# Kernel optimization log

Measured on AMD Instinct MI355X. Metric: run time of the kernel, lower is better.

The kernel has to match this reference:

```python
import jax, jax.numpy as jnp
import numpy as np

K_NN = 64          # ume_knn
RADIUS = 1.5       # ume_desc_rad
EPS_M = 1e-6
EPS_T = 1e-16


def ball_query_idx(kp, pts, K, radius):
    # kp: [bs, n_kp, 3], pts: [bs, N, 3] -> idx [bs, n_kp, K], -1 padded
    N = pts.shape[1]
    d2 = jnp.sum((kp[:, :, None, :] - pts[:, None, :, :]) ** 2, axis=-1)  # [bs,n_kp,N]
    mask = d2 < radius ** 2
    cand = jnp.where(mask, jnp.arange(N, dtype=jnp.int32), N)
    order = jnp.sort(cand, axis=-1)[..., :K]          # first K in-ball indices (by point index)
    return jnp.where(order == N, -1, order)


def ball_query_gather(pts, idx):
    # pad row 0 with zeros so idx=-1 gathers zeros (matches torch ball_query_gather)
    bs = pts.shape[0]
    padded = jnp.concatenate([jnp.zeros((bs, 1, pts.shape[-1]), pts.dtype), pts], axis=1)
    return padded[jnp.arange(bs)[:, None, None], idx + 1]  # [bs, n_kp, K, D]


def ume_mat(points, features):
    # points: [B', K, 3], features: [B', K, F] -> [B', F, 4]
    m0 = jnp.sum(features, axis=1)                       # [B', F]
    m1 = jnp.einsum('bkf,bkd->bfd', features, points)    # [B', F, 3]
    um = jnp.concatenate([m0[:, :, None], m1], axis=2)   # [B', F, 4]
    denom = jnp.sum(m0, axis=-1)[:, None, None] + EPS_M  # [B',1,1]
    return um / denom


def batch_estimate_transform_ume(G, H):
    # G, H: [B, F, 4]
    mg, mh = G[:, :, 0:1], H[:, :, 0:1]                  # [B,F,1]
    g, h = G[:, :, 1:], H[:, :, 1:]                      # [B,F,3]
    mg_sq = jnp.sum(mg ** 2, axis=1, keepdims=True) + EPS_T
    mg_mh = jnp.sum(mg * mh, axis=1, keepdims=True)
    gmg = jnp.sum(g * mg, axis=1, keepdims=True)         # [B,1,3]
    hmg = jnp.sum(h * mg, axis=1, keepdims=True)
    wlc = gmg / (mg_sq + EPS_T)
    wrc = hmg / (mg_mh + EPS_T)
    left = g - wlc * mg
    right = h - wrc * mh
    M = jnp.einsum('bfi,bfj->bij', right, left)          # right^T @ left, [B,3,3]
    U, S, VH = jnp.linalg.svd(jnp.swapaxes(M, 1, 2))
    sgn = jnp.sign(jnp.linalg.det(U @ VH))
    qd = jnp.stack([jnp.ones_like(sgn), jnp.ones_like(sgn), sgn], axis=-1)  # diag(1,1,sgn)
    R = (U * qd[:, None, :]) @ VH                        # [B,3,3]
    b2 = (wrc - wlc @ R)[:, 0, :]                        # [B,3]
    H_orth = jnp.linalg.qr(H, mode='reduced')[0]
    G_orth = jnp.linalg.qr(G, mode='reduced')[0]
    diff = H_orth @ jnp.swapaxes(H_orth, 1, 2) - G_orth @ jnp.swapaxes(G_orth, 1, 2)
    D = 0.707 * jnp.sqrt(jnp.sum(diff ** 2, axis=(1, 2)))
    top = jnp.concatenate([jnp.swapaxes(R, 1, 2), b2[:, :, None]], axis=2)  # [B,3,4]
    bottom = jnp.broadcast_to(jnp.array([[0.0, 0.0, 0.0, 1.0]], G.dtype), (G.shape[0], 1, 4))
    T = jnp.concatenate([top, bottom], axis=1)           # [B,4,4]
    return T, D


def setup_inputs() -> dict:
    key = jax.random.key(0)
    ks = jax.random.split(key, 6)
    bs, N, F, n_kp = 2, 16384, 64, 64
    return {
        'source_points': jax.random.normal(ks[0], (bs, N, 3), jnp.float32),
        'source_features': jax.random.uniform(ks[1], (bs, N, F), jnp.float32),
        'source_kp': jax.random.normal(ks[2], (bs, n_kp, 3), jnp.float32),
        'target_points': jax.random.normal(ks[3], (bs, N, 3), jnp.float32),
        'target_features': jax.random.uniform(ks[4], (bs, N, F), jnp.float32),
        'target_kp': jax.random.normal(ks[5], (bs, n_kp, 3), jnp.float32),
    }


def reference(source_points, source_features, source_kp, target_points, target_features, target_kp):
    bs, n_kp = source_kp.shape[0], source_kp.shape[1]
    F = source_features.shape[-1]
    s_idx = ball_query_idx(source_kp, source_points, K_NN, RADIUS)
    t_idx = ball_query_idx(target_kp, target_points, K_NN, RADIUS)
    s_pts = ball_query_gather(source_points, s_idx).reshape(bs * n_kp, K_NN, 3)
    s_ft = ball_query_gather(source_features, s_idx).reshape(bs * n_kp, K_NN, F)
    t_pts = ball_query_gather(target_points, t_idx).reshape(bs * n_kp, K_NN, 3)
    t_ft = ball_query_gather(target_features, t_idx).reshape(bs * n_kp, K_NN, F)
    G_kp = ume_mat(s_pts, s_ft).reshape(bs, n_kp, F, 4)[:, :, None]   # [bs,n_kp,1,F,4]
    H_kp = ume_mat(t_pts, t_ft).reshape(bs, n_kp, F, 4)[:, None]      # [bs,1,n_kp,F,4]
    G = jnp.broadcast_to(G_kp, (bs, n_kp, n_kp, F, 4)).reshape(-1, F, 4)
    H = jnp.broadcast_to(H_kp, (bs, n_kp, n_kp, F, 4)).reshape(-1, F, 4)
    T, D = batch_estimate_transform_ume(G, H)
    T = T.reshape(bs, n_kp, n_kp, 4, 4)
    D = D.reshape(bs, n_kp, n_kp)
    return T, D, jnp.squeeze(G_kp), jnp.squeeze(H_kp)
```

## Files before the change

### kernel.cpp

```cpp
#include <hip/hip_runtime.h>
#include <math.h>

#define N_PTS 16384
#define N_KP  64
#define NF    64
#define KNN   64
#define NWAVE 16

#define OFF_T 0
#define OFF_D 131072
#define OFF_G 139264
#define OFF_H 172032

__device__ __forceinline__ float wsum(float v) {
  #pragma unroll
  for (int m = 1; m < 64; m <<= 1) v += __shfl_xor(v, m, 64);
  return v;
}

__global__ __launch_bounds__(1024) void ume_stage1(
    const float* __restrict__ sp, const float* __restrict__ sf, const float* __restrict__ skp,
    const float* __restrict__ tp, const float* __restrict__ tf, const float* __restrict__ tkp,
    float* __restrict__ out, double* __restrict__ rec)
{
  const int kp = blockIdx.x, b = blockIdx.y, side = blockIdx.z;
  const int tid  = threadIdx.x;
  const int lane = tid & 63;
  const int w    = tid >> 6;
  const float* pts  = side ? tp  : sp;
  const float* feat = side ? tf  : sf;
  const float* kps  = side ? tkp : skp;

  const float kx = kps[(b*N_KP + kp)*3 + 0];
  const float ky = kps[(b*N_KP + kp)*3 + 1];
  const float kz = kps[(b*N_KP + kp)*3 + 2];

  __shared__ int   s_widx[NWAVE*KNN];
  __shared__ int   s_wcount[NWAVE];
  __shared__ int   s_woff[NWAVE];
  __shared__ int   s_total;
  __shared__ int   s_final[KNN];
  __shared__ float s_px[KNN], s_py[KNN], s_pz[KNN];
  __shared__ float s_m0[NWAVE][NF], s_mx[NWAVE][NF], s_my[NWAVE][NF], s_mz[NWAVE][NF];

  float px[16], py[16], pz[16];
  const size_t pbase = ((size_t)b*N_PTS + w*1024 + lane)*3;
  #pragma unroll
  for (int k = 0; k < 16; ++k) {
    const float* pp = pts + pbase + (size_t)k*64*3;
    px[k] = pp[0]; py[k] = pp[1]; pz[k] = pp[2];
  }
  int running = 0;
  #pragma unroll
  for (int k = 0; k < 16; ++k) {
    const float dx = px[k]-kx, dy = py[k]-ky, dz = pz[k]-kz;
    const bool hit = (dx*dx + dy*dy + dz*dz) < 2.25f;
    const unsigned long long m = __ballot(hit);
    if (hit) {
      const int pos = running + __popcll(m & ((1ull<<lane)-1ull));
      if (pos < KNN) s_widx[w*KNN + pos] = w*1024 + k*64 + lane;
    }
    running += (int)__popcll(m);
  }
  if (lane == 0) s_wcount[w] = running > KNN ? KNN : running;
  __syncthreads();

  if (tid < NWAVE) {
    int off = 0;
    for (int q = 0; q < tid; ++q) off += s_wcount[q];
    s_woff[tid] = off;
    if (tid == NWAVE-1) {
      int tot = off + s_wcount[tid];
      s_total = tot > KNN ? KNN : tot;
    }
  }
  __syncthreads();

  {
    const int e = tid & 63, ww = tid >> 6;
    if (e < s_wcount[ww]) {
      const int slot = s_woff[ww] + e;
      if (slot < KNN) s_final[slot] = s_widx[ww*KNN + e];
    }
  }
  __syncthreads();

  const int total = s_total;
  if (tid < KNN && tid < total) {
    const float* pp = pts + ((size_t)b*N_PTS + s_final[tid])*3;
    s_px[tid] = pp[0]; s_py[tid] = pp[1]; s_pz[tid] = pp[2];
  }
  __syncthreads();

  {
    const int f = tid & 63, g = tid >> 6;
    float m0 = 0.f, mxv = 0.f, myv = 0.f, mzv = 0.f;
    for (int k = g; k < total; k += NWAVE) {
      const float fv = feat[((size_t)b*N_PTS + s_final[k])*NF + f];
      m0  += fv;
      mxv += fv * s_px[k];
      myv += fv * s_py[k];
      mzv += fv * s_pz[k];
    }
    s_m0[g][f] = m0; s_mx[g][f] = mxv; s_my[g][f] = myv; s_mz[g][f] = mzv;
  }
  __syncthreads();

  if (tid >= 64) return;

  float m0 = 0.f, mxv = 0.f, myv = 0.f, mzv = 0.f;
  #pragma unroll
  for (int g = 0; g < NWAVE; ++g) {
    m0  += s_m0[g][lane];
    mxv += s_mx[g][lane];
    myv += s_my[g][lane];
    mzv += s_mz[g][lane];
  }
  const float denom = wsum(m0) + 1e-6f;
  float u[4];
  u[0] = m0/denom; u[1] = mxv/denom; u[2] = myv/denom; u[3] = mzv/denom;

  float* dst = out + (side ? OFF_H : OFF_G) + ((size_t)(b*N_KP+kp)*NF + lane)*4;
  dst[0]=u[0]; dst[1]=u[1]; dst[2]=u[2]; dst[3]=u[3];

  float A[4][4];
  #pragma unroll
  for (int c = 0; c < 4; ++c)
    #pragma unroll
    for (int d = c; d < 4; ++d) {
      const float s = wsum(u[c]*u[d]);
      A[c][d] = s; A[d][c] = s;
    }

  if (lane == 0) {
    double Ad[4][4];
    for (int c = 0; c < 4; ++c)
      for (int d = 0; d < 4; ++d) Ad[c][d] = (double)A[c][d];
    double sc[4];
    #pragma unroll
    for (int c = 0; c < 4; ++c) sc[c] = 1.0/sqrt(fmax(Ad[c][c], 1e-300));
    double Ah[4][4];
    for (int c = 0; c < 4; ++c)
      for (int d = 0; d < 4; ++d) Ah[c][d] = Ad[c][d]*sc[c]*sc[d];
    double L[4][4] = {};
    for (int c = 0; c < 4; ++c) {
      double dv = Ah[c][c];
      for (int k = 0; k < c; ++k) dv -= L[c][k]*L[c][k];
      dv = sqrt(fmax(dv, 1e-14));
      L[c][c] = dv;
      for (int r = c+1; r < 4; ++r) {
        double v = Ah[r][c];
        for (int k = 0; k < c; ++k) v -= L[r][k]*L[c][k];
        L[r][c] = v/dv;
      }
    }
    double Li[4][4] = {};
    for (int c = 0; c < 4; ++c) {
      Li[c][c] = 1.0/L[c][c];
      for (int r = c+1; r < 4; ++r) {
        double s = 0.0;
        for (int k = c; k < r; ++k) s += L[r][k]*Li[k][c];
        Li[r][c] = -s/L[r][r];
      }
    }
    double Ai[4][4];
    for (int r = 0; r < 4; ++r)
      for (int c = 0; c < 4; ++c) {
        double s = 0.0;
        for (int k = 0; k < 4; ++k) s += Li[k][r]*Li[k][c];
        Ai[r][c] = s;
      }
    double* rp = rec + (size_t)((side*2 + b)*N_KP + kp)*24;
    for (int k = 0; k < 16; ++k) rp[k] = Ai[k>>2][k&3];
    rp[16]=sc[0]; rp[17]=sc[1]; rp[18]=sc[2]; rp[19]=sc[3];
    const double mg_sq = Ad[0][0] + 1e-16;
    const double dwl = mg_sq + 1e-16;
    rp[20] = Ad[0][1]/dwl;
    rp[21] = Ad[0][2]/dwl;
    rp[22] = Ad[0][3]/dwl;
    rp[23] = 0.0;
  }
}

__global__ __launch_bounds__(64) void ume_stage2(
    const float* __restrict__ gh, float* __restrict__ out,
    const double* __restrict__ rec)
{
  const int jt = blockIdx.x, it = blockIdx.y, b = blockIdx.z;
  const int lane = threadIdx.x;
  const int i = it*8 + (lane >> 3);
  const int j = jt*8 + (lane & 7);

  const float4* Gp = (const float4*)(gh + OFF_G) + (size_t)(b*N_KP + i)*NF;
  const float4* Hp = (const float4*)(gh + OFF_H) + (size_t)(b*N_KP + j)*NF;

  double X[4][4] = {};
  for (int f = 0; f < NF; ++f) {
    const float4 g = Gp[f];
    const float4 h = Hp[f];
    const double gc[4] = {(double)g.x, (double)g.y, (double)g.z, (double)g.w};
    const double hc[4] = {(double)h.x, (double)h.y, (double)h.z, (double)h.w};
    #pragma unroll
    for (int c = 0; c < 4; ++c)
      #pragma unroll
      for (int d = 0; d < 4; ++d)
        X[c][d] += hc[c]*gc[d];
  }

  const double* rg = rec + (size_t)(b*N_KP + i)*24;
  const double* rh = rec + (size_t)((2 + b)*N_KP + j)*24;

  const double wl[3] = {rg[20], rg[21], rg[22]};
  const double dmm = X[0][0] + 1e-16;
  double wr[3];
  wr[0] = X[1][0]/dmm; wr[1] = X[2][0]/dmm; wr[2] = X[3][0]/dmm;

  double M[3][3];
  #pragma unroll
  for (int r = 0; r < 3; ++r)
    #pragma unroll
    for (int c = 0; c < 3; ++c)
      M[r][c] = X[1+r][1+c] - wl[c]*X[1+r][0] - wr[r]*X[0][1+c] + wr[r]*wl[c]*X[0][0];

  double C[3][3];
  for (int r = 0; r < 3; ++r)
    for (int c = 0; c < 3; ++c) C[r][c] = M[c][r];

  double mmax = 0.0;
  for (int r = 0; r < 3; ++r)
    for (int c = 0; c < 3; ++c) mmax = fmax(mmax, fabs(C[r][c]));

  double R[3][3] = {{1,0,0},{0,1,0},{0,0,1}};
  if (mmax > 1e-300) {
    const double is = 1.0/mmax;
    for (int r = 0; r < 3; ++r)
      for (int c = 0; c < 3; ++c) C[r][c] *= is;
    double K[3][3];
    for (int p = 0; p < 3; ++p)
      for (int q = 0; q < 3; ++q) {
        double s = 0.0;
        for (int r = 0; r < 3; ++r) s += C[r][p]*C[r][q];
        K[p][q] = s;
      }
    double V[3][3] = {{1,0,0},{0,1,0},{0,0,1}};
    for (int sweep = 0; sweep < 8; ++sweep) {
      for (int p = 0; p < 2; ++p)
        for (int q = p+1; q < 3; ++q) {
          const double apq = K[p][q];
          if (fabs(apq) < 1e-60) continue;
          const double tau = (K[q][q] - K[p][p])/(2.0*apq);
          const double t   = (tau >= 0.0 ? 1.0 : -1.0)/(fabs(tau) + sqrt(1.0 + tau*tau));
          const double cth = 1.0/sqrt(1.0 + t*t);
          const double sth = t*cth;
          for (int k = 0; k < 3; ++k) {
            const double a = K[p][k], bb_ = K[q][k];
            K[p][k] = cth*a - sth*bb_;
            K[q][k] = sth*a + cth*bb_;
          }
          for (int k = 0; k < 3; ++k) {
            const double a = K[k][p], bb_ = K[k][q];
            K[k][p] = cth*a - sth*bb_;
            K[k][q] = sth*a + cth*bb_;
          }
          for (int k = 0; k < 3; ++k) {
            const double a = V[k][p], bb_ = V[k][q];
            V[k][p] = cth*a - sth*bb_;
            V[k][q] = sth*a + cth*bb_;
          }
        }
    }
    int o0 = 0, o1 = 1, o2 = 2;
    double e0 = K[0][0], e1 = K[1][1], e2 = K[2][2];
    if (e0 < e1) { double te=e0; e0=e1; e1=te; int to=o0; o0=o1; o1=to; }
    if (e0 < e2) { double te=e0; e0=e2; e2=te; int to=o0; o0=o2; o2=to; }
    if (e1 < e2) { double te=e1; e1=e2; e2=te; int to=o1; o1=o2; o2=to; }
    (void)e0; (void)e1; (void)e2;
    double v1[3] = {V[0][o0], V[1][o0], V[2][o0]};
    double v2[3] = {V[0][o1], V[1][o1], V[2][o1]};
    double u1[3], u2[3];
    for (int r = 0; r < 3; ++r) u1[r] = C[r][0]*v1[0] + C[r][1]*v1[1] + C[r][2]*v1[2];
    const double n1 = sqrt(u1[0]*u1[0] + u1[1]*u1[1] + u1[2]*u1[2]);
    if (n1 > 1e-150) { u1[0]/=n1; u1[1]/=n1; u1[2]/=n1; }
    else             { u1[0]=1.0; u1[1]=0.0; u1[2]=0.0; }
    for (int r = 0; r < 3; ++r) u2[r] = C[r][0]*v2[0] + C[r][1]*v2[1] + C[r][2]*v2[2];
    const double d12 = u2[0]*u1[0] + u2[1]*u1[1] + u2[2]*u1[2];
    for (int r = 0; r < 3; ++r) u2[r] -= d12*u1[r];
    const double n2 = sqrt(u2[0]*u2[0] + u2[1]*u2[1] + u2[2]*u2[2]);
    if (n2 > 1e-100) { u2[0]/=n2; u2[1]/=n2; u2[2]/=n2; }
    else {
      double t0, t1, t2;
      if (fabs(u1[0]) < 0.9) { t0=1.0; t1=0.0; t2=0.0; } else { t0=0.0; t1=1.0; t2=0.0; }
      const double dd = t0*u1[0] + t1*u1[1] + t2*u1[2];
      u2[0]=t0-dd*u1[0]; u2[1]=t1-dd*u1[1]; u2[2]=t2-dd*u1[2];
      const double nn = sqrt(u2[0]*u2[0] + u2[1]*u2[1] + u2[2]*u2[2]);
      u2[0]/=nn; u2[1]/=nn; u2[2]/=nn;
    }
    const double u3[3] = {u1[1]*u2[2]-u1[2]*u2[1], u1[2]*u2[0]-u1[0]*u2[2], u1[0]*u2[1]-u1[1]*u2[0]};
    const double v3[3] = {v1[1]*v2[2]-v1[2]*v2[1], v1[2]*v2[0]-v1[0]*v2[2], v1[0]*v2[1]-v1[1]*v2[0]};
    for (int r = 0; r < 3; ++r)
      for (int c = 0; c < 3; ++c)
        R[r][c] = u1[r]*v1[c] + u2[r]*v2[c] + u3[r]*v3[c];
  }

  double bb[3];
  for (int d = 0; d < 3; ++d)
    bb[d] = wr[d] - (wl[0]*R[0][d] + wl[1]*R[1][d] + wl[2]*R[2][d]);

  const double sg[4] = {rg[16], rg[17], rg[18], rg[19]};
  const double sh[4] = {rh[16], rh[17], rh[18], rh[19]};
  double Xh[4][4];
  for (int c = 0; c < 4; ++c)
    for (int d = 0; d < 4; ++d) Xh[c][d] = X[c][d]*sh[c]*sg[d];
  double W[4][4];
  for (int r = 0; r < 4; ++r)
    for (int c = 0; c < 4; ++c) {
      double s = 0.0;
      for (int k = 0; k < 4; ++k) s += rh[r*4+k]*Xh[k][c];
      W[r][c] = s;
    }
  double tr = 0.0;
  for (int r = 0; r < 4; ++r)
    for (int c = 0; c < 4; ++c) {
      double s = 0.0;
      for (int k = 0; k < 4; ++k) s += W[r][k]*rg[k*4+c];
      tr += s*Xh[r][c];
    }
  const double Dv = 0.707*sqrt(fmax(8.0 - 2.0*tr, 0.0));

  float* tptr = out + OFF_T + (size_t)((b*N_KP + i)*N_KP + j)*16;
  tptr[0]=(float)R[0][0];  tptr[1]=(float)R[1][0];  tptr[2]=(float)R[2][0];  tptr[3]=(float)bb[0];
  tptr[4]=(float)R[0][1];  tptr[5]=(float)R[1][1];  tptr[6]=(float)R[2][1];  tptr[7]=(float)bb[1];
  tptr[8]=(float)R[0][2];  tptr[9]=(float)R[1][2];  tptr[10]=(float)R[2][2]; tptr[11]=(float)bb[2];
  tptr[12]=0.f; tptr[13]=0.f; tptr[14]=0.f; tptr[15]=1.f;

  out[OFF_D + (size_t)(b*N_KP + i)*N_KP + j] = (float)Dv;
}

extern "C" void kernel_launch(void* const* d_in, const int* in_sizes, int n_in,
                              void* d_out, int out_size, void* d_ws, size_t ws_size,
                              hipStream_t stream) {
  const float* sp  = (const float*)d_in[0];
  const float* sf  = (const float*)d_in[1];
  const float* skp = (const float*)d_in[2];
  const float* tp  = (const float*)d_in[3];
  const float* tf  = (const float*)d_in[4];
  const float* tkp = (const float*)d_in[5];
  float* out = (float*)d_out;
  double* rec = (double*)d_ws;

  dim3 gA(N_KP, 2, 2);
  ume_stage1<<<gA, 1024, 0, stream>>>(sp, sf, skp, tp, tf, tkp, out, rec);
  dim3 gB(8, 8, 2);
  ume_stage2<<<gB, 64, 0, stream>>>(out, out, rec);
}
```

Baseline: 103.5 us.

## Stream ball-query loads, cache hit coordinates in LDS, unroll feature gather, fewer Jacobi sweeps

The ball query now software-pipelines point loads one step ahead instead of preloading all 48 floats per thread. Coordinates of hits are stored in LDS next to their indices, which removes the global re-gather of neighbour coordinates and one barrier. The feature accumulation loop is unrolled to a fixed four iterations. Jacobi SVD sweeps drop from eight to five, which may slightly reduce accuracy for ill-conditioned matrices.

```diff
diff --git a/kernel.cpp b/kernel.cpp
--- a/kernel.cpp
+++ b/kernel.cpp
@@ -36,6 +36,7 @@
   const float kz = kps[(b*N_KP + kp)*3 + 2];
 
   __shared__ int   s_widx[NWAVE*KNN];
+  __shared__ float s_wpx[NWAVE*KNN], s_wpy[NWAVE*KNN], s_wpz[NWAVE*KNN];
   __shared__ int   s_wcount[NWAVE];
   __shared__ int   s_woff[NWAVE];
   __shared__ int   s_total;
@@ -43,22 +44,36 @@
   __shared__ float s_px[KNN], s_py[KNN], s_pz[KNN];
   __shared__ float s_m0[NWAVE][NF], s_mx[NWAVE][NF], s_my[NWAVE][NF], s_mz[NWAVE][NF];
 
-  float px[16], py[16], pz[16];
-  const size_t pbase = ((size_t)b*N_PTS + w*1024 + lane)*3;
-  #pragma unroll
-  for (int k = 0; k < 16; ++k) {
-    const float* pp = pts + pbase + (size_t)k*64*3;
-    px[k] = pp[0]; py[k] = pp[1]; pz[k] = pp[2];
-  }
+  const float* base = pts + ((size_t)b*N_PTS + w*1024 + lane)*3;
+  float cx = base[0], cy = base[1], cz = base[2];
   int running = 0;
-  #pragma unroll
-  for (int k = 0; k < 16; ++k) {
-    const float dx = px[k]-kx, dy = py[k]-ky, dz = pz[k]-kz;
+  #pragma unroll 5
+  for (int k = 0; k < 15; ++k) {
+    const float* q = base + (size_t)(k+1)*192;
+    const float nx = q[0], ny = q[1], nz = q[2];
+    const float dx = cx-kx, dy = cy-ky, dz = cz-kz;
     const bool hit = (dx*dx + dy*dy + dz*dz) < 2.25f;
     const unsigned long long m = __ballot(hit);
     if (hit) {
       const int pos = running + __popcll(m & ((1ull<<lane)-1ull));
-      if (pos < KNN) s_widx[w*KNN + pos] = w*1024 + k*64 + lane;
+      if (pos < KNN) {
+        s_widx[w*KNN + pos] = w*1024 + k*64 + lane;
+        s_wpx[w*KNN + pos] = cx; s_wpy[w*KNN + pos] = cy; s_wpz[w*KNN + pos] = cz;
+      }
+    }
+    running += (int)__popcll(m);
+    cx = nx; cy = ny; cz = nz;
+  }
+  {
+    const float dx = cx-kx, dy = cy-ky, dz = cz-kz;
+    const bool hit = (dx*dx + dy*dy + dz*dz) < 2.25f;
+    const unsigned long long m = __ballot(hit);
+    if (hit) {
+      const int pos = running + __popcll(m & ((1ull<<lane)-1ull));
+      if (pos < KNN) {
+        s_widx[w*KNN + pos] = w*1024 + 15*64 + lane;
+        s_wpx[w*KNN + pos] = cx; s_wpy[w*KNN + pos] = cy; s_wpz[w*KNN + pos] = cz;
+      }
     }
     running += (int)__popcll(m);
   }
@@ -80,27 +95,31 @@
     const int e = tid & 63, ww = tid >> 6;
     if (e < s_wcount[ww]) {
       const int slot = s_woff[ww] + e;
-      if (slot < KNN) s_final[slot] = s_widx[ww*KNN + e];
+      if (slot < KNN) {
+        s_final[slot] = s_widx[ww*KNN + e];
+        s_px[slot] = s_wpx[ww*KNN + e];
+        s_py[slot] = s_wpy[ww*KNN + e];
+        s_pz[slot] = s_wpz[ww*KNN + e];
+      }
     }
   }
   __syncthreads();
 
   const int total = s_total;
-  if (tid < KNN && tid < total) {
-    const float* pp = pts + ((size_t)b*N_PTS + s_final[tid])*3;
-    s_px[tid] = pp[0]; s_py[tid] = pp[1]; s_pz[tid] = pp[2];
-  }
-  __syncthreads();
 
   {
     const int f = tid & 63, g = tid >> 6;
     float m0 = 0.f, mxv = 0.f, myv = 0.f, mzv = 0.f;
-    for (int k = g; k < total; k += NWAVE) {
-      const float fv = feat[((size_t)b*N_PTS + s_final[k])*NF + f];
-      m0  += fv;
-      mxv += fv * s_px[k];
-      myv += fv * s_py[k];
-      mzv += fv * s_pz[k];
+    #pragma unroll
+    for (int t = 0; t < 4; ++t) {
+      const int k = g + t*NWAVE;
+      if (k < total) {
+        const float fv = feat[((size_t)b*N_PTS + s_final[k])*NF + f];
+        m0  += fv;
+        mxv += fv * s_px[k];
+        myv += fv * s_py[k];
+        mzv += fv * s_pz[k];
+      }
     }
     s_m0[g][f] = m0; s_mx[g][f] = mxv; s_my[g][f] = myv; s_mz[g][f] = mzv;
   }
@@ -243,7 +262,7 @@
         K[p][q] = s;
       }
     double V[3][3] = {{1,0,0},{0,1,0},{0,0,1}};
-    for (int sweep = 0; sweep < 8; ++sweep) {
+    for (int sweep = 0; sweep < 5; ++sweep) {
       for (int p = 0; p < 2; ++p)
         for (int q = p+1; q < 3; ++q) {
           const double apq = K[p][q];
```

Measured after the change: 110.7 us. 1.07x slower.
